# Performance work log

Hardware: AMD Instinct MI355X
Metric: run time of the kernel (lower is better)

## Reference

```python
import jax, jax.numpy as jnp
import numpy as np

B, S, E, H = 2, 2048, 1024, 16
D = E // H  # head_dim = 64


def setup_inputs() -> dict:
    key = jax.random.key(0)
    ks = jax.random.split(key, 11)
    s = 1.0 / np.sqrt(E)
    return {
        "query": jax.random.normal(ks[0], (B, S, E), jnp.float32),
        "key":   jax.random.normal(ks[1], (B, S, E), jnp.float32),
        "value": jax.random.normal(ks[2], (B, S, E), jnp.float32),
        "q_w": jax.random.uniform(ks[3], (E, E), jnp.float32, -s, s),
        "q_b": jax.random.uniform(ks[4], (E,), jnp.float32, -s, s),
        "k_w": jax.random.uniform(ks[5], (E, E), jnp.float32, -s, s),
        "k_b": jax.random.uniform(ks[6], (E,), jnp.float32, -s, s),
        "v_w": jax.random.uniform(ks[7], (E, E), jnp.float32, -s, s),
        "v_b": jax.random.uniform(ks[8], (E,), jnp.float32, -s, s),
        "o_w": jax.random.uniform(ks[9], (E, E), jnp.float32, -s, s),
        "o_b": jax.random.uniform(ks[10], (E,), jnp.float32, -s, s),
    }


def reference(query, key, value, q_w, q_b, k_w, k_b, v_w, v_b, o_w, o_b):
    b, sq, _ = query.shape
    sk = key.shape[1]
    # linear projections (torch Linear: x @ W.T + b)
    Q = (query @ q_w.T + q_b).reshape(b, sq, H, D).transpose(0, 2, 1, 3)  # b h sq d
    K = (key   @ k_w.T + k_b).reshape(b, sk, H, D).transpose(0, 2, 1, 3)
    V = (value @ v_w.T + v_b).reshape(b, sk, H, D).transpose(0, 2, 1, 3)
    scores = jnp.einsum("bhqd,bhkd->bhqk", Q, K) / jnp.sqrt(jnp.float32(D))
    attn = jax.nn.softmax(scores, axis=-1)
    out = jnp.einsum("bhqk,bhkd->bhqd", attn, V)  # b h sq d
    out = out.transpose(0, 2, 1, 3).reshape(b, sq, E)
    return out @ o_w.T + o_b
```

## Files before the change

### kernel.cpp

```cpp
#include <hip/hip_runtime.h>
#include <stdint.h>

typedef __bf16 bf16x8 __attribute__((ext_vector_type(8)));
typedef short short8 __attribute__((ext_vector_type(8)));
typedef float f32x4 __attribute__((ext_vector_type(4)));
typedef float f32x16 __attribute__((ext_vector_type(16)));
typedef unsigned short u16;
typedef unsigned int u32;

#define MROWS 4096
#define EDIM  1024
#define SQ    2048
#define DH    64

#if __has_builtin(__builtin_amdgcn_exp2f)
#define EXP2(x) __builtin_amdgcn_exp2f(x)
#else
#define EXP2(x) exp2f(x)
#endif

__device__ __forceinline__ u16 f2bf(float f) {
  unsigned u = __builtin_bit_cast(unsigned, f);
  return (u16)((u + 0x7FFFu + ((u >> 16) & 1u)) >> 16);
}

__device__ __forceinline__ u32 cvtpk_bf16(float lo, float hi) {
  u32 r;
  asm("v_cvt_pk_bf16_f32 %0, %1, %2" : "=v"(r) : "v"(lo), "v"(hi));
  return r;
}
__device__ __forceinline__ void swap32(u32& a, u32& b) {
  asm("v_permlane32_swap_b32 %0, %1" : "+v"(a), "+v"(b));
}

__global__ __launch_bounds__(256) void cvt7_kernel(
    const float* __restrict__ s0, const float* __restrict__ s1,
    const float* __restrict__ s2, const float* __restrict__ s3,
    const float* __restrict__ s4, const float* __restrict__ s5,
    const float* __restrict__ s6,
    u16* __restrict__ d0, u16* __restrict__ d1, u16* __restrict__ d2,
    u16* __restrict__ d3, u16* __restrict__ d4, u16* __restrict__ d5,
    u16* __restrict__ d6, int nact, int nw) {
  const float* s; u16* d; int n;
  switch (blockIdx.y) {
    case 0: s = s0; d = d0; n = nact; break;
    case 1: s = s1; d = d1; n = nact; break;
    case 2: s = s2; d = d2; n = nact; break;
    case 3: s = s3; d = d3; n = nw; break;
    case 4: s = s4; d = d4; n = nw; break;
    case 5: s = s5; d = d5; n = nw; break;
    default: s = s6; d = d6; n = nw; break;
  }
  int i = (blockIdx.x * 256 + threadIdx.x) * 8;
  if (i >= n) return;
  float4 a = *(const float4*)(s + i);
  float4 b = *(const float4*)(s + i + 4);
  short8 r;
  r[0] = (short)f2bf(a.x); r[1] = (short)f2bf(a.y);
  r[2] = (short)f2bf(a.z); r[3] = (short)f2bf(a.w);
  r[4] = (short)f2bf(b.x); r[5] = (short)f2bf(b.y);
  r[6] = (short)f2bf(b.z); r[7] = (short)f2bf(b.w);
  *(short8*)(d + i) = r;
}

template <int OUT_F32>
__device__ __forceinline__ void gemm_core(
    const u16* __restrict__ A, const u16* __restrict__ W,
    const float* __restrict__ bias, void* __restrict__ C,
    int m0, int n0, u16* As, u16* Bs) {
  const int tid = threadIdx.x, lane = tid & 63, w = tid >> 6;
  const int r = lane & 15, g = lane >> 4;
  const int wr = w >> 1, wc = w & 1;
  f32x4 acc[4][4] = {};

  for (int kt = 0; kt < 32; ++kt) {
    const int k0 = kt * 32;
    __syncthreads();
#pragma unroll
    for (int i = 0; i < 2; ++i) {
      int c = i * 256 + tid;
      int row = c >> 2, ko = (c & 3) * 8;
      __builtin_amdgcn_global_load_lds(
          (const __attribute__((address_space(1))) void*)(A + (size_t)(m0 + row) * EDIM + k0 + ko),
          (__attribute__((address_space(3))) void*)(As + (i * 256 + w * 64) * 8), 16, 0, 0);
      __builtin_amdgcn_global_load_lds(
          (const __attribute__((address_space(1))) void*)(W + (size_t)(n0 + row) * EDIM + k0 + ko),
          (__attribute__((address_space(3))) void*)(Bs + (i * 256 + w * 64) * 8), 16, 0, 0);
    }
    __syncthreads();
    bf16x8 af[4], bfv[4];
#pragma unroll
    for (int i = 0; i < 4; ++i) {
      af[i]  = *(const bf16x8*)&As[(wr * 64 + i * 16 + r) * 32 + g * 8];
      bfv[i] = *(const bf16x8*)&Bs[(wc * 64 + i * 16 + r) * 32 + g * 8];
    }
#pragma unroll
    for (int mi = 0; mi < 4; ++mi)
#pragma unroll
      for (int ni = 0; ni < 4; ++ni)
        acc[mi][ni] = __builtin_amdgcn_mfma_f32_16x16x32_bf16(af[mi], bfv[ni], acc[mi][ni], 0, 0, 0);
  }
#pragma unroll
  for (int ni = 0; ni < 4; ++ni) {
    const int col = n0 + wc * 64 + ni * 16 + r;
    const float bv = bias[col];
#pragma unroll
    for (int mi = 0; mi < 4; ++mi) {
#pragma unroll
      for (int rr = 0; rr < 4; ++rr) {
        const int rowm = m0 + wr * 64 + mi * 16 + g * 4 + rr;
        float v = acc[mi][ni][rr] + bv;
        if (OUT_F32) ((float*)C)[(size_t)rowm * EDIM + col] = v;
        else ((u16*)C)[(size_t)rowm * EDIM + col] = f2bf(v);
      }
    }
  }
}

__global__ __launch_bounds__(256) void gemm_qkv(
    const u16* __restrict__ X0, const u16* __restrict__ X1, const u16* __restrict__ X2,
    const u16* __restrict__ W0, const u16* __restrict__ W1, const u16* __restrict__ W2,
    const float* __restrict__ b0, const float* __restrict__ b1, const float* __restrict__ b2,
    u16* __restrict__ C0, u16* __restrict__ C1, u16* __restrict__ C2) {
  __shared__ u16 As[128 * 32];
  __shared__ u16 Bs[128 * 32];
  const u16 *A, *W; const float* bias; u16* C;
  switch (blockIdx.z) {
    case 0: A = X0; W = W0; bias = b0; C = C0; break;
    case 1: A = X1; W = W1; bias = b1; C = C1; break;
    default: A = X2; W = W2; bias = b2; C = C2; break;
  }
  gemm_core<0>(A, W, bias, C, blockIdx.y * 128, blockIdx.x * 128, As, Bs);
}

__global__ __launch_bounds__(256) void gemm_oproj(
    const u16* __restrict__ A, const u16* __restrict__ W,
    const float* __restrict__ bias, float* __restrict__ C) {
  __shared__ u16 As[128 * 32];
  __shared__ u16 Bs[128 * 32];
  gemm_core<1>(A, W, bias, C, blockIdx.y * 128, blockIdx.x * 128, As, Bs);
}

__device__ __forceinline__ void k_stage(const u16* __restrict__ Kg, int kt, int tid,
                                        int w, u16* kb) {
#pragma unroll
  for (int ri = 0; ri < 2; ++ri) {
    int idx = ri * 256 + tid, row = idx >> 3, sl = idx & 7;
    __builtin_amdgcn_global_load_lds(
        (const __attribute__((address_space(1))) void*)(
            Kg + (size_t)(kt * 64 + row) * EDIM + ((sl ^ (row & 7)) * 8)),
        (__attribute__((address_space(3))) void*)(kb + (ri * 256 + w * 64) * 8), 16, 0, 0);
  }
}

__device__ __forceinline__ void v_issue(const u16* __restrict__ Vg, int kt, int tid,
                                        u32* vdw) {
  const int vd0 = (tid & 31) * 2, kvc = tid >> 5;
#pragma unroll
  for (int j = 0; j < 8; ++j)
    vdw[j] = *(const u32*)(Vg + (size_t)(kt * 64 + kvc * 8 + j) * EDIM + vd0);
}

__device__ __forceinline__ void v_write(u16* vt, int tid, const u32* vdw) {
  const int vd0 = (tid & 31) * 2, kvc = tid >> 5;
  union { u32 u[4]; short8 s; } lo8, hi8;
#pragma unroll
  for (int i = 0; i < 4; ++i) {
    lo8.u[i] = (vdw[2 * i] & 0xFFFFu) | (vdw[2 * i + 1] << 16);
    hi8.u[i] = (vdw[2 * i] >> 16) | (vdw[2 * i + 1] & 0xFFFF0000u);
  }
  const int sl = kvc ^ (vd0 & 7);
  *(short8*)&vt[vd0 * 64 + sl * 8] = lo8.s;
  *(short8*)&vt[(vd0 + 1) * 64 + (sl ^ 1) * 8] = hi8.s;
}

#define CE_CONST 0.18033688011112042f

__device__ __forceinline__ void qk_step(f32x16 (&st)[2], const u16* kb,
                                        const bf16x8 (&qf)[4], const int (&colA)[4],
                                        int lq) {
  __builtin_amdgcn_s_setprio(1);
#pragma unroll
  for (int t = 0; t < 2; ++t) {
    f32x16 z = {};
#pragma unroll
    for (int f = 0; f < 4; ++f) {
      const bf16x8 ka = *(const bf16x8*)&kb[(t * 32 + lq) * 64 + colA[f]];
      z = __builtin_amdgcn_mfma_f32_32x32x16_bf16(ka, qf[f], z, 0, 0, 0);
    }
    st[t] = z;
  }
  __builtin_amdgcn_s_setprio(0);
}

__device__ __forceinline__ void softmax_pb(f32x16 (&st)[2], float& m, float& l,
                                           f32x16 (&accO)[2], bf16x8 (&pb)[4]) {
  float mx[16];
#pragma unroll
  for (int i = 0; i < 16; ++i) mx[i] = fmaxf(st[0][i], st[1][i]);
#pragma unroll
  for (int s = 8; s >= 1; s >>= 1)
#pragma unroll
    for (int i = 0; i < s; ++i) mx[i] = fmaxf(mx[i], mx[i + s]);
  float vm = mx[0];
  vm = fmaxf(vm, __shfl_xor(vm, 32));
  if (!__all(vm <= m + 8.0f)) {
    const float mn = fmaxf(m, vm);
    const float scl = EXP2((m - mn) * CE_CONST);
    m = mn;
    l *= scl;
#pragma unroll
    for (int dt = 0; dt < 2; ++dt)
#pragma unroll
      for (int rr = 0; rr < 16; ++rr) accO[dt][rr] *= scl;
  }
  const float mc = m * CE_CONST;
#pragma unroll
  for (int t = 0; t < 2; ++t)
#pragma unroll
    for (int rr = 0; rr < 16; ++rr)
      st[t][rr] = EXP2(st[t][rr] * CE_CONST - mc);
  float sm[16];
#pragma unroll
  for (int i = 0; i < 16; ++i) sm[i] = st[0][i] + st[1][i];
#pragma unroll
  for (int s = 8; s >= 1; s >>= 1)
#pragma unroll
    for (int i = 0; i < s; ++i) sm[i] = sm[i] + sm[i + s];
  float ts = sm[0];
  ts += __shfl_xor(ts, 32);
  l += ts;
#pragma unroll
  for (int t = 0; t < 2; ++t)
#pragma unroll
    for (int kh = 0; kh < 2; ++kh) {
      const int rb = kh * 8;
      u32 a0 = cvtpk_bf16(st[t][rb + 0], st[t][rb + 1]);
      u32 b0 = cvtpk_bf16(st[t][rb + 4], st[t][rb + 5]);
      swap32(a0, b0);
      u32 a1 = cvtpk_bf16(st[t][rb + 2], st[t][rb + 3]);
      u32 b1 = cvtpk_bf16(st[t][rb + 6], st[t][rb + 7]);
      swap32(a1, b1);
      union { u32 u[4]; bf16x8 v; } pu;
      pu.u[0] = a0; pu.u[1] = a1; pu.u[2] = b0; pu.u[3] = b1;
      pb[t * 2 + kh] = pu.v;
    }
}

__device__ __forceinline__ void pv_step(f32x16 (&accO)[2], const bf16x8 (&pb)[4],
                                        const u16* vt, const int (&colA)[4], int lq) {
  __builtin_amdgcn_s_setprio(1);
#pragma unroll
  for (int dt = 0; dt < 2; ++dt)
#pragma unroll
    for (int ks = 0; ks < 4; ++ks) {
      const bf16x8 va = *(const bf16x8*)&vt[(dt * 32 + lq) * 64 + colA[ks]];
      accO[dt] = __builtin_amdgcn_mfma_f32_32x32x16_bf16(va, pb[ks], accO[dt], 0, 0, 0);
    }
  __builtin_amdgcn_s_setprio(0);
}

__global__ __launch_bounds__(256) void attn2_kernel(
    const u16* __restrict__ Q, const u16* __restrict__ K,
    const u16* __restrict__ V, u16* __restrict__ O) {
  __shared__ __align__(16) u16 KB[2][64 * 64];
  __shared__ __align__(16) u16 VT[3][64 * 64];
  const int tid = threadIdx.x, lane = tid & 63, w = tid >> 6;
  const int lq = lane & 31, hi = lane >> 5;
  const int bid = blockIdx.x;
  const int b2 = (bid & 7) * 64 + (bid >> 3);
  const int qb = b2 & 15, bh = b2 >> 4;
  const int b = bh >> 4, h = bh & 15;
  const u16* Qg = Q + (size_t)b * SQ * EDIM + h * DH;
  const u16* Kg = K + (size_t)b * SQ * EDIM + h * DH;
  const u16* Vg = V + (size_t)b * SQ * EDIM + h * DH;
  const int q0 = qb * 128 + w * 32;

  bf16x8 qf[4];
#pragma unroll
  for (int f = 0; f < 4; ++f)
    qf[f] = *(const bf16x8*)(Qg + (size_t)(q0 + lq) * EDIM + f * 16 + hi * 8);

  const int swz = (lq & 7) << 4;
  int colA[4];
#pragma unroll
  for (int f = 0; f < 4; ++f) colA[f] = ((f * 32 + hi * 16) ^ swz) >> 1;

  f32x16 accO[2] = {};
  f32x16 stA[2], stB[2];
  bf16x8 pb[4];
  float m = -3e38f, l = 0.f;
  u32 vdw[8];

  k_stage(Kg, 0, tid, w, KB[0]);
  v_issue(Vg, 0, tid, vdw);
  v_write(VT[0], tid, vdw);
  __syncthreads();
  k_stage(Kg, 1, tid, w, KB[1]);
  v_issue(Vg, 1, tid, vdw);
  qk_step(stA, KB[0], qf, colA, lq);
  v_write(VT[1], tid, vdw);
  __syncthreads();

#define ATTN_BODY(T, SP, SN)                                                  \
  {                                                                           \
    if ((T) < 31) { k_stage(Kg, (T) + 1, tid, w, KB[((T) + 1) & 1]);          \
                    v_issue(Vg, (T) + 1, tid, vdw); }                         \
    qk_step(SN, KB[(T) & 1], qf, colA, lq);                                   \
    softmax_pb(SP, m, l, accO, pb);                                           \
    pv_step(accO, pb, VT[((T) - 1) % 3], colA, lq);                           \
    if ((T) < 31) v_write(VT[((T) + 1) % 3], tid, vdw);                       \
    __syncthreads();                                                          \
  }

  for (int t = 1; t < 31; t += 2) {
    ATTN_BODY(t, stA, stB);
    ATTN_BODY(t + 1, stB, stA);
  }
  ATTN_BODY(31, stA, stB);
#undef ATTN_BODY

  softmax_pb(stB, m, l, accO, pb);
  pv_step(accO, pb, VT[31 % 3], colA, lq);

  const float rinv = 1.0f / l;
  u16* Ost = (u16*)KB;
#pragma unroll
  for (int dt = 0; dt < 2; ++dt)
#pragma unroll
    for (int rr = 0; rr < 16; ++rr) {
      const int d = dt * 32 + (rr & 3) + 8 * (rr >> 2) + 4 * hi;
      Ost[w * 2048 + lq * 64 + (d ^ ((lq & 7) << 3))] = f2bf(accO[dt][rr] * rinv);
    }
  __syncthreads();
#pragma unroll
  for (int ri = 0; ri < 4; ++ri) {
    const int idx = ri * 256 + tid;
    const int w2 = idx >> 8, q = (idx >> 3) & 31, c = idx & 7;
    short8 o = *(const short8*)&Ost[w2 * 2048 + q * 64 + ((c ^ (q & 7)) * 8)];
    *(short8*)(O + (size_t)(b * SQ + qb * 128 + w2 * 32 + q) * EDIM + h * DH + c * 8) = o;
  }
}

extern "C" void kernel_launch(void* const* d_in, const int* in_sizes, int n_in,
                              void* d_out, int out_size, void* d_ws, size_t ws_size,
                              hipStream_t stream) {
  (void)in_sizes; (void)n_in; (void)out_size; (void)ws_size;
  const float* query = (const float*)d_in[0];
  const float* key   = (const float*)d_in[1];
  const float* value = (const float*)d_in[2];
  const float* q_w = (const float*)d_in[3];
  const float* q_b = (const float*)d_in[4];
  const float* k_w = (const float*)d_in[5];
  const float* k_b = (const float*)d_in[6];
  const float* v_w = (const float*)d_in[7];
  const float* v_b = (const float*)d_in[8];
  const float* o_w = (const float*)d_in[9];
  const float* o_b = (const float*)d_in[10];

  u16* ws = (u16*)d_ws;
  const size_t NX = (size_t)MROWS * EDIM;
  const size_t NW = (size_t)EDIM * EDIM;
  u16* Xq = ws;
  u16* Xk = Xq + NX;
  u16* Xv = Xk + NX;
  u16* Wq = Xv + NX;
  u16* Wk = Wq + NW;
  u16* Wv = Wk + NW;
  u16* Wo = Wv + NW;
  u16* Qp = Wo + NW;
  u16* Kp = Qp + NX;
  u16* Vp = Kp + NX;
  u16* At = Xq;

  cvt7_kernel<<<dim3((int)(NX / 8 / 256), 7), 256, 0, stream>>>(
      query, key, value, q_w, k_w, v_w, o_w,
      Xq, Xk, Xv, Wq, Wk, Wv, Wo, (int)NX, (int)NW);

  gemm_qkv<<<dim3(8, 32, 3), 256, 0, stream>>>(
      Xq, Xk, Xv, Wq, Wk, Wv, q_b, k_b, v_b, Qp, Kp, Vp);

  attn2_kernel<<<512, 256, 0, stream>>>(Qp, Kp, Vp, At);

  gemm_oproj<<<dim3(8, 32), 256, 0, stream>>>(At, Wo, o_b, (float*)d_out);
}
```

Baseline: 138.4 us.

## Widen attention KV tile to 128 and drop the QK/softmax software pipeline

The attention kernel now processes 128 keys per iteration instead of 64, with K and V^T buffers double-buffered at the larger size. The previous three-stage pipeline, which overlapped QK of the next tile with softmax and PV of the previous one, is replaced by a simple per-tile loop: QK, softmax, PV. The goal is to halve the number of barriers and loop iterations and to amortize the softmax reductions over more keys. In exchange it loses the overlap between QK MFMAs and softmax VALU work, and it raises register pressure (16 vdw, 4 score tiles, 8 P fragments) and LDS use.

```diff
diff --git a/kernel.cpp b/kernel.cpp
--- a/kernel.cpp
+++ b/kernel.cpp
@@ -144,11 +144,11 @@
 __device__ __forceinline__ void k_stage(const u16* __restrict__ Kg, int kt, int tid,
                                         int w, u16* kb) {
 #pragma unroll
-  for (int ri = 0; ri < 2; ++ri) {
+  for (int ri = 0; ri < 4; ++ri) {
     int idx = ri * 256 + tid, row = idx >> 3, sl = idx & 7;
     __builtin_amdgcn_global_load_lds(
         (const __attribute__((address_space(1))) void*)(
-            Kg + (size_t)(kt * 64 + row) * EDIM + ((sl ^ (row & 7)) * 8)),
+            Kg + (size_t)(kt * 128 + row) * EDIM + ((sl ^ (row & 7)) * 8)),
         (__attribute__((address_space(3))) void*)(kb + (ri * 256 + w * 64) * 8), 16, 0, 0);
   }
 }
@@ -157,114 +157,35 @@
                                         u32* vdw) {
   const int vd0 = (tid & 31) * 2, kvc = tid >> 5;
 #pragma unroll
-  for (int j = 0; j < 8; ++j)
-    vdw[j] = *(const u32*)(Vg + (size_t)(kt * 64 + kvc * 8 + j) * EDIM + vd0);
+  for (int j = 0; j < 16; ++j)
+    vdw[j] = *(const u32*)(Vg + (size_t)(kt * 128 + kvc * 16 + j) * EDIM + vd0);
 }
 
 __device__ __forceinline__ void v_write(u16* vt, int tid, const u32* vdw) {
   const int vd0 = (tid & 31) * 2, kvc = tid >> 5;
-  union { u32 u[4]; short8 s; } lo8, hi8;
+  union { u32 u[4]; short8 s; } a0, a1, c0, c1;
 #pragma unroll
   for (int i = 0; i < 4; ++i) {
-    lo8.u[i] = (vdw[2 * i] & 0xFFFFu) | (vdw[2 * i + 1] << 16);
-    hi8.u[i] = (vdw[2 * i] >> 16) | (vdw[2 * i + 1] & 0xFFFF0000u);
-  }
-  const int sl = kvc ^ (vd0 & 7);
-  *(short8*)&vt[vd0 * 64 + sl * 8] = lo8.s;
-  *(short8*)&vt[(vd0 + 1) * 64 + (sl ^ 1) * 8] = hi8.s;
+    a0.u[i] = (vdw[2 * i] & 0xFFFFu) | (vdw[2 * i + 1] << 16);
+    c0.u[i] = (vdw[2 * i] >> 16) | (vdw[2 * i + 1] & 0xFFFF0000u);
+    a1.u[i] = (vdw[8 + 2 * i] & 0xFFFFu) | (vdw[8 + 2 * i + 1] << 16);
+    c1.u[i] = (vdw[8 + 2 * i] >> 16) | (vdw[8 + 2 * i + 1] & 0xFFFF0000u);
+  }
+  const int s0 = (kvc * 2) ^ (vd0 & 7), s1 = (kvc * 2 + 1) ^ (vd0 & 7);
+  const int s2 = (kvc * 2) ^ ((vd0 + 1) & 7), s3 = (kvc * 2 + 1) ^ ((vd0 + 1) & 7);
+  *(short8*)&vt[vd0 * 128 + s0 * 8] = a0.s;
+  *(short8*)&vt[vd0 * 128 + s1 * 8] = a1.s;
+  *(short8*)&vt[(vd0 + 1) * 128 + s2 * 8] = c0.s;
+  *(short8*)&vt[(vd0 + 1) * 128 + s3 * 8] = c1.s;
 }
 
 #define CE_CONST 0.18033688011112042f
-
-__device__ __forceinline__ void qk_step(f32x16 (&st)[2], const u16* kb,
-                                        const bf16x8 (&qf)[4], const int (&colA)[4],
-                                        int lq) {
-  __builtin_amdgcn_s_setprio(1);
-#pragma unroll
-  for (int t = 0; t < 2; ++t) {
-    f32x16 z = {};
-#pragma unroll
-    for (int f = 0; f < 4; ++f) {
-      const bf16x8 ka = *(const bf16x8*)&kb[(t * 32 + lq) * 64 + colA[f]];
-      z = __builtin_amdgcn_mfma_f32_32x32x16_bf16(ka, qf[f], z, 0, 0, 0);
-    }
-    st[t] = z;
-  }
-  __builtin_amdgcn_s_setprio(0);
-}
-
-__device__ __forceinline__ void softmax_pb(f32x16 (&st)[2], float& m, float& l,
-                                           f32x16 (&accO)[2], bf16x8 (&pb)[4]) {
-  float mx[16];
-#pragma unroll
-  for (int i = 0; i < 16; ++i) mx[i] = fmaxf(st[0][i], st[1][i]);
-#pragma unroll
-  for (int s = 8; s >= 1; s >>= 1)
-#pragma unroll
-    for (int i = 0; i < s; ++i) mx[i] = fmaxf(mx[i], mx[i + s]);
-  float vm = mx[0];
-  vm = fmaxf(vm, __shfl_xor(vm, 32));
-  if (!__all(vm <= m + 8.0f)) {
-    const float mn = fmaxf(m, vm);
-    const float scl = EXP2((m - mn) * CE_CONST);
-    m = mn;
-    l *= scl;
-#pragma unroll
-    for (int dt = 0; dt < 2; ++dt)
-#pragma unroll
-      for (int rr = 0; rr < 16; ++rr) accO[dt][rr] *= scl;
-  }
-  const float mc = m * CE_CONST;
-#pragma unroll
-  for (int t = 0; t < 2; ++t)
-#pragma unroll
-    for (int rr = 0; rr < 16; ++rr)
-      st[t][rr] = EXP2(st[t][rr] * CE_CONST - mc);
-  float sm[16];
-#pragma unroll
-  for (int i = 0; i < 16; ++i) sm[i] = st[0][i] + st[1][i];
-#pragma unroll
-  for (int s = 8; s >= 1; s >>= 1)
-#pragma unroll
-    for (int i = 0; i < s; ++i) sm[i] = sm[i] + sm[i + s];
-  float ts = sm[0];
-  ts += __shfl_xor(ts, 32);
-  l += ts;
-#pragma unroll
-  for (int t = 0; t < 2; ++t)
-#pragma unroll
-    for (int kh = 0; kh < 2; ++kh) {
-      const int rb = kh * 8;
-      u32 a0 = cvtpk_bf16(st[t][rb + 0], st[t][rb + 1]);
-      u32 b0 = cvtpk_bf16(st[t][rb + 4], st[t][rb + 5]);
-      swap32(a0, b0);
-      u32 a1 = cvtpk_bf16(st[t][rb + 2], st[t][rb + 3]);
-      u32 b1 = cvtpk_bf16(st[t][rb + 6], st[t][rb + 7]);
-      swap32(a1, b1);
-      union { u32 u[4]; bf16x8 v; } pu;
-      pu.u[0] = a0; pu.u[1] = a1; pu.u[2] = b0; pu.u[3] = b1;
-      pb[t * 2 + kh] = pu.v;
-    }
-}
-
-__device__ __forceinline__ void pv_step(f32x16 (&accO)[2], const bf16x8 (&pb)[4],
-                                        const u16* vt, const int (&colA)[4], int lq) {
-  __builtin_amdgcn_s_setprio(1);
-#pragma unroll
-  for (int dt = 0; dt < 2; ++dt)
-#pragma unroll
-    for (int ks = 0; ks < 4; ++ks) {
-      const bf16x8 va = *(const bf16x8*)&vt[(dt * 32 + lq) * 64 + colA[ks]];
-      accO[dt] = __builtin_amdgcn_mfma_f32_32x32x16_bf16(va, pb[ks], accO[dt], 0, 0, 0);
-    }
-  __builtin_amdgcn_s_setprio(0);
-}
 
 __global__ __launch_bounds__(256) void attn2_kernel(
     const u16* __restrict__ Q, const u16* __restrict__ K,
     const u16* __restrict__ V, u16* __restrict__ O) {
-  __shared__ __align__(16) u16 KB[2][64 * 64];
-  __shared__ __align__(16) u16 VT[3][64 * 64];
+  __shared__ __align__(16) u16 KB[2][128 * 64];
+  __shared__ __align__(16) u16 VT[2][64 * 128];
   const int tid = threadIdx.x, lane = tid & 63, w = tid >> 6;
   const int lq = lane & 31, hi = lane >> 5;
   const int bid = blockIdx.x;
@@ -285,43 +206,110 @@
   int colA[4];
 #pragma unroll
   for (int f = 0; f < 4; ++f) colA[f] = ((f * 32 + hi * 16) ^ swz) >> 1;
+  int colV[8];
+#pragma unroll
+  for (int c = 0; c < 8; ++c) colV[c] = ((c * 32 + hi * 16) ^ swz) >> 1;
 
   f32x16 accO[2] = {};
-  f32x16 stA[2], stB[2];
-  bf16x8 pb[4];
+  f32x16 st[4];
+  bf16x8 pb[8];
   float m = -3e38f, l = 0.f;
-  u32 vdw[8];
+  u32 vdw[16];
 
   k_stage(Kg, 0, tid, w, KB[0]);
   v_issue(Vg, 0, tid, vdw);
   v_write(VT[0], tid, vdw);
   __syncthreads();
-  k_stage(Kg, 1, tid, w, KB[1]);
-  v_issue(Vg, 1, tid, vdw);
-  qk_step(stA, KB[0], qf, colA, lq);
-  v_write(VT[1], tid, vdw);
-  __syncthreads();
-
-#define ATTN_BODY(T, SP, SN)                                                  \
-  {                                                                           \
-    if ((T) < 31) { k_stage(Kg, (T) + 1, tid, w, KB[((T) + 1) & 1]);          \
-                    v_issue(Vg, (T) + 1, tid, vdw); }                         \
-    qk_step(SN, KB[(T) & 1], qf, colA, lq);                                   \
-    softmax_pb(SP, m, l, accO, pb);                                           \
-    pv_step(accO, pb, VT[((T) - 1) % 3], colA, lq);                           \
-    if ((T) < 31) v_write(VT[((T) + 1) % 3], tid, vdw);                       \
-    __syncthreads();                                                          \
-  }
-
-  for (int t = 1; t < 31; t += 2) {
-    ATTN_BODY(t, stA, stB);
-    ATTN_BODY(t + 1, stB, stA);
-  }
-  ATTN_BODY(31, stA, stB);
-#undef ATTN_BODY
-
-  softmax_pb(stB, m, l, accO, pb);
-  pv_step(accO, pb, VT[31 % 3], colA, lq);
+
+  for (int P = 0; P < 16; ++P) {
+    const int cur = P & 1;
+    if (P < 15) {
+      k_stage(Kg, P + 1, tid, w, KB[cur ^ 1]);
+      v_issue(Vg, P + 1, tid, vdw);
+    }
+
+    __builtin_amdgcn_s_setprio(1);
+#pragma unroll
+    for (int tt = 0; tt < 4; ++tt) {
+      f32x16 z = {};
+#pragma unroll
+      for (int f = 0; f < 4; ++f) {
+        const bf16x8 ka = *(const bf16x8*)&KB[cur][(tt * 32 + lq) * 64 + colA[f]];
+        z = __builtin_amdgcn_mfma_f32_32x32x16_bf16(ka, qf[f], z, 0, 0, 0);
+      }
+      st[tt] = z;
+    }
+    __builtin_amdgcn_s_setprio(0);
+
+    {
+      float mx[16];
+#pragma unroll
+      for (int i = 0; i < 16; ++i)
+        mx[i] = fmaxf(fmaxf(st[0][i], st[1][i]), fmaxf(st[2][i], st[3][i]));
+#pragma unroll
+      for (int s = 8; s >= 1; s >>= 1)
+#pragma unroll
+        for (int i = 0; i < s; ++i) mx[i] = fmaxf(mx[i], mx[i + s]);
+      float vm = mx[0];
+      vm = fmaxf(vm, __shfl_xor(vm, 32));
+      if (!__all(vm <= m + 8.0f)) {
+        const float mn = fmaxf(m, vm);
+        const float scl = EXP2((m - mn) * CE_CONST);
+        m = mn;
+        l *= scl;
+#pragma unroll
+        for (int dt = 0; dt < 2; ++dt)
+#pragma unroll
+          for (int rr = 0; rr < 16; ++rr) accO[dt][rr] *= scl;
+      }
+      const float mc = m * CE_CONST;
+#pragma unroll
+      for (int tt = 0; tt < 4; ++tt)
+#pragma unroll
+        for (int rr = 0; rr < 16; ++rr)
+          st[tt][rr] = EXP2(st[tt][rr] * CE_CONST - mc);
+      float sm[16];
+#pragma unroll
+      for (int i = 0; i < 16; ++i)
+        sm[i] = (st[0][i] + st[1][i]) + (st[2][i] + st[3][i]);
+#pragma unroll
+      for (int s = 8; s >= 1; s >>= 1)
+#pragma unroll
+        for (int i = 0; i < s; ++i) sm[i] = sm[i] + sm[i + s];
+      float ts = sm[0];
+      ts += __shfl_xor(ts, 32);
+      l += ts;
+    }
+
+#pragma unroll
+    for (int tt = 0; tt < 4; ++tt)
+#pragma unroll
+      for (int kh = 0; kh < 2; ++kh) {
+        const int rb = kh * 8;
+        u32 a0 = cvtpk_bf16(st[tt][rb + 0], st[tt][rb + 1]);
+        u32 b0 = cvtpk_bf16(st[tt][rb + 4], st[tt][rb + 5]);
+        swap32(a0, b0);
+        u32 a1 = cvtpk_bf16(st[tt][rb + 2], st[tt][rb + 3]);
+        u32 b1 = cvtpk_bf16(st[tt][rb + 6], st[tt][rb + 7]);
+        swap32(a1, b1);
+        union { u32 u[4]; bf16x8 v; } pu;
+        pu.u[0] = a0; pu.u[1] = a1; pu.u[2] = b0; pu.u[3] = b1;
+        pb[tt * 2 + kh] = pu.v;
+      }
+
+    __builtin_amdgcn_s_setprio(1);
+#pragma unroll
+    for (int dt = 0; dt < 2; ++dt)
+#pragma unroll
+      for (int c = 0; c < 8; ++c) {
+        const bf16x8 va = *(const bf16x8*)&VT[cur][(dt * 32 + lq) * 128 + colV[c]];
+        accO[dt] = __builtin_amdgcn_mfma_f32_32x32x16_bf16(va, pb[c], accO[dt], 0, 0, 0);
+      }
+    __builtin_amdgcn_s_setprio(0);
+
+    if (P < 15) v_write(VT[cur ^ 1], tid, vdw);
+    __syncthreads();
+  }
 
   const float rinv = 1.0f / l;
   u16* Ost = (u16*)KB;
```

Result: no change. 137.0 us (-1.0%).

## Split attention KV range across two warp groups and merge softmax states in LDS

Applied to the files above, without the earlier changes.

The attention kernel now runs 512 threads per block, with two groups of four waves. Each group processes half of the key/value sequence for the same 128 queries using its own K/V LDS buffers. At the end, group 1 writes its partial accumulators and (m, l) statistics to LDS, and group 0 rescales and merges them before normalising and storing. This raises per-block parallelism and halves the serial KV loop length, at the cost of doubled LDS usage, extra merge traffic and synchronisation, and possible occupancy limits from the larger block.

```diff
diff --git a/kernel.cpp b/kernel.cpp
--- a/kernel.cpp
+++ b/kernel.cpp
@@ -141,28 +141,28 @@
   gemm_core<1>(A, W, bias, C, blockIdx.y * 128, blockIdx.x * 128, As, Bs);
 }
 
-__device__ __forceinline__ void k_stage(const u16* __restrict__ Kg, int kt, int tid,
-                                        int w, u16* kb) {
+__device__ __forceinline__ void k_stage(const u16* __restrict__ Kg, int kt, int lt,
+                                        int lw, u16* kb) {
 #pragma unroll
   for (int ri = 0; ri < 2; ++ri) {
-    int idx = ri * 256 + tid, row = idx >> 3, sl = idx & 7;
+    int idx = ri * 256 + lt, row = idx >> 3, sl = idx & 7;
     __builtin_amdgcn_global_load_lds(
         (const __attribute__((address_space(1))) void*)(
             Kg + (size_t)(kt * 64 + row) * EDIM + ((sl ^ (row & 7)) * 8)),
-        (__attribute__((address_space(3))) void*)(kb + (ri * 256 + w * 64) * 8), 16, 0, 0);
-  }
-}
-
-__device__ __forceinline__ void v_issue(const u16* __restrict__ Vg, int kt, int tid,
+        (__attribute__((address_space(3))) void*)(kb + (ri * 256 + lw * 64) * 8), 16, 0, 0);
+  }
+}
+
+__device__ __forceinline__ void v_issue(const u16* __restrict__ Vg, int kt, int lt,
                                         u32* vdw) {
-  const int vd0 = (tid & 31) * 2, kvc = tid >> 5;
+  const int vd0 = (lt & 31) * 2, kvc = lt >> 5;
 #pragma unroll
   for (int j = 0; j < 8; ++j)
     vdw[j] = *(const u32*)(Vg + (size_t)(kt * 64 + kvc * 8 + j) * EDIM + vd0);
 }
 
-__device__ __forceinline__ void v_write(u16* vt, int tid, const u32* vdw) {
-  const int vd0 = (tid & 31) * 2, kvc = tid >> 5;
+__device__ __forceinline__ void v_write(u16* vt, int lt, const u32* vdw) {
+  const int vd0 = (lt & 31) * 2, kvc = lt >> 5;
   union { u32 u[4]; short8 s; } lo8, hi8;
 #pragma unroll
   for (int i = 0; i < 4; ++i) {
@@ -260,21 +260,22 @@
   __builtin_amdgcn_s_setprio(0);
 }
 
-__global__ __launch_bounds__(256) void attn2_kernel(
+__global__ __launch_bounds__(512) void attn2_kernel(
     const u16* __restrict__ Q, const u16* __restrict__ K,
     const u16* __restrict__ V, u16* __restrict__ O) {
-  __shared__ __align__(16) u16 KB[2][64 * 64];
-  __shared__ __align__(16) u16 VT[3][64 * 64];
+  __shared__ __align__(16) u16 KB[2][2][64 * 64];
+  __shared__ __align__(16) u16 VT[2][3][64 * 64];
   const int tid = threadIdx.x, lane = tid & 63, w = tid >> 6;
+  const int sp = w >> 2, qw = w & 3, lt = tid & 255;
   const int lq = lane & 31, hi = lane >> 5;
   const int bid = blockIdx.x;
   const int b2 = (bid & 7) * 64 + (bid >> 3);
   const int qb = b2 & 15, bh = b2 >> 4;
   const int b = bh >> 4, h = bh & 15;
   const u16* Qg = Q + (size_t)b * SQ * EDIM + h * DH;
-  const u16* Kg = K + (size_t)b * SQ * EDIM + h * DH;
-  const u16* Vg = V + (size_t)b * SQ * EDIM + h * DH;
-  const int q0 = qb * 128 + w * 32;
+  const u16* Kg = K + (size_t)b * SQ * EDIM + h * DH + (size_t)sp * 1024 * EDIM;
+  const u16* Vg = V + (size_t)b * SQ * EDIM + h * DH + (size_t)sp * 1024 * EDIM;
+  const int q0 = qb * 128 + qw * 32;
 
   bf16x8 qf[4];
 #pragma unroll
@@ -292,50 +293,87 @@
   float m = -3e38f, l = 0.f;
   u32 vdw[8];
 
-  k_stage(Kg, 0, tid, w, KB[0]);
-  v_issue(Vg, 0, tid, vdw);
-  v_write(VT[0], tid, vdw);
-  __syncthreads();
-  k_stage(Kg, 1, tid, w, KB[1]);
-  v_issue(Vg, 1, tid, vdw);
-  qk_step(stA, KB[0], qf, colA, lq);
-  v_write(VT[1], tid, vdw);
+  k_stage(Kg, 0, lt, qw, KB[sp][0]);
+  v_issue(Vg, 0, lt, vdw);
+  v_write(VT[sp][0], lt, vdw);
+  __syncthreads();
+  k_stage(Kg, 1, lt, qw, KB[sp][1]);
+  v_issue(Vg, 1, lt, vdw);
+  qk_step(stA, KB[sp][0], qf, colA, lq);
+  v_write(VT[sp][1], lt, vdw);
   __syncthreads();
 
 #define ATTN_BODY(T, SP, SN)                                                  \
   {                                                                           \
-    if ((T) < 31) { k_stage(Kg, (T) + 1, tid, w, KB[((T) + 1) & 1]);          \
-                    v_issue(Vg, (T) + 1, tid, vdw); }                         \
-    qk_step(SN, KB[(T) & 1], qf, colA, lq);                                   \
+    if ((T) < 15) { k_stage(Kg, (T) + 1, lt, qw, KB[sp][((T) + 1) & 1]);      \
+                    v_issue(Vg, (T) + 1, lt, vdw); }                          \
+    qk_step(SN, KB[sp][(T) & 1], qf, colA, lq);                               \
     softmax_pb(SP, m, l, accO, pb);                                           \
-    pv_step(accO, pb, VT[((T) - 1) % 3], colA, lq);                           \
-    if ((T) < 31) v_write(VT[((T) + 1) % 3], tid, vdw);                       \
+    pv_step(accO, pb, VT[sp][((T) - 1) % 3], colA, lq);                       \
+    if ((T) < 15) v_write(VT[sp][((T) + 1) % 3], lt, vdw);                    \
     __syncthreads();                                                          \
   }
 
-  for (int t = 1; t < 31; t += 2) {
+  for (int t = 1; t < 15; t += 2) {
     ATTN_BODY(t, stA, stB);
     ATTN_BODY(t + 1, stB, stA);
   }
-  ATTN_BODY(31, stA, stB);
+  ATTN_BODY(15, stA, stB);
 #undef ATTN_BODY
 
   softmax_pb(stB, m, l, accO, pb);
-  pv_step(accO, pb, VT[31 % 3], colA, lq);
-
-  const float rinv = 1.0f / l;
+  pv_step(accO, pb, VT[sp][15 % 3], colA, lq);
+  __syncthreads();
+
+  float* mrgf = (float*)&KB[0][0][0];
+  float* sttf = (float*)&VT[0][0][0];
+  if (sp == 1) {
+#pragma unroll
+    for (int dt = 0; dt < 2; ++dt)
+#pragma unroll
+      for (int rr = 0; rr < 16; ++rr) {
+        const int d = dt * 32 + (rr & 3) + 8 * (rr >> 2) + 4 * hi;
+        mrgf[(qw * 32 + lq) * 64 + ((d + 2 * lq) & 63)] = accO[dt][rr];
+      }
+    if (lane < 32) {
+      sttf[(qw * 32 + lq) * 2 + 0] = m;
+      sttf[(qw * 32 + lq) * 2 + 1] = l;
+    }
+  }
+  __syncthreads();
+  if (sp == 0) {
+    const float m1 = sttf[(qw * 32 + lq) * 2 + 0];
+    const float l1 = sttf[(qw * 32 + lq) * 2 + 1];
+    const float ms = fmaxf(m, m1);
+    const float e0 = EXP2((m - ms) * CE_CONST);
+    const float e1 = EXP2((m1 - ms) * CE_CONST);
+    l = l * e0 + l1 * e1;
+#pragma unroll
+    for (int dt = 0; dt < 2; ++dt)
+#pragma unroll
+      for (int rr = 0; rr < 16; ++rr) {
+        const int d = dt * 32 + (rr & 3) + 8 * (rr >> 2) + 4 * hi;
+        accO[dt][rr] = accO[dt][rr] * e0 +
+                       mrgf[(qw * 32 + lq) * 64 + ((d + 2 * lq) & 63)] * e1;
+      }
+  }
+  __syncthreads();
+
   u16* Ost = (u16*)KB;
-#pragma unroll
-  for (int dt = 0; dt < 2; ++dt)
-#pragma unroll
-    for (int rr = 0; rr < 16; ++rr) {
-      const int d = dt * 32 + (rr & 3) + 8 * (rr >> 2) + 4 * hi;
-      Ost[w * 2048 + lq * 64 + (d ^ ((lq & 7) << 3))] = f2bf(accO[dt][rr] * rinv);
-    }
-  __syncthreads();
-#pragma unroll
-  for (int ri = 0; ri < 4; ++ri) {
-    const int idx = ri * 256 + tid;
+  if (sp == 0) {
+    const float rinv = 1.0f / l;
+#pragma unroll
+    for (int dt = 0; dt < 2; ++dt)
+#pragma unroll
+      for (int rr = 0; rr < 16; ++rr) {
+        const int d = dt * 32 + (rr & 3) + 8 * (rr >> 2) + 4 * hi;
+        Ost[qw * 2048 + lq * 64 + (d ^ ((lq & 7) << 3))] = f2bf(accO[dt][rr] * rinv);
+      }
+  }
+  __syncthreads();
+#pragma unroll
+  for (int ri = 0; ri < 2; ++ri) {
+    const int idx = ri * 512 + tid;
     const int w2 = idx >> 8, q = (idx >> 3) & 31, c = idx & 7;
     short8 o = *(const short8*)&Ost[w2 * 2048 + q * 64 + ((c ^ (q & 7)) * 8)];
     *(short8*)(O + (size_t)(b * SQ + qb * 128 + w2 * 32 + q) * EDIM + h * DH + c * 8) = o;
@@ -380,7 +418,7 @@
   gemm_qkv<<<dim3(8, 32, 3), 256, 0, stream>>>(
       Xq, Xk, Xv, Wq, Wk, Wv, q_b, k_b, v_b, Qp, Kp, Vp);
 
-  attn2_kernel<<<512, 256, 0, stream>>>(Qp, Kp, Vp, At);
+  attn2_kernel<<<512, 512, 0, stream>>>(Qp, Kp, Vp, At);
 
   gemm_oproj<<<dim3(8, 32), 256, 0, stream>>>(At, Wo, o_b, (float*)d_out);
 }
```

Result: slower. 141.8 us (+2.4%).
